# Performance work log

Hardware: AMD Instinct MI355X
Metric: run time of the kernel (lower is better)

## Reference

```python
import jax, jax.numpy as jnp
import numpy as np
from jax import lax

B, EMB, HEADS, HD, LAYERS, FIX, ADAPT, MLP, NCLS = 32, 768, 12, 64, 12, 6, 6, 3072, 100
PE_N, PE_D = 100, 256
SCALE = 1.0 / np.sqrt(HD)


def _ln(x, g, b, eps=1e-5):
    m = jnp.mean(x, axis=-1, keepdims=True)
    v = jnp.mean((x - m) ** 2, axis=-1, keepdims=True)
    return (x - m) / jnp.sqrt(v + eps) * g + b


def _vit_block(x, g1, b1, qkvw, qkvb, pw, pb, g2, b2, f1w, f1b, f2w, f2b):
    Bn, N, _ = x.shape
    h = _ln(x, g1, b1)
    qkv = (h @ qkvw + qkvb).reshape(Bn, N, 3, HEADS, HD)
    q, k, v = [qkv[:, :, i].transpose(0, 2, 1, 3) for i in range(3)]  # [B,H,N,hd]
    attn = jax.nn.softmax(jnp.einsum('bhqd,bhkd->bhqk', q, k) * SCALE, axis=-1)
    o = jnp.einsum('bhqk,bhkd->bhqd', attn, v).transpose(0, 2, 1, 3).reshape(Bn, N, EMB)
    x = x + (o @ pw + pb)
    h = _ln(x, g2, b2)
    return x + (jax.nn.gelu(h @ f1w + f1b, approximate=False) @ f2w + f2b)


def _sinusoid_table():
    pos = np.arange(PE_N)[:, None].astype(np.float64)
    j = np.arange(PE_D)[None, :]
    ang = pos / np.power(10000.0, 2 * (j // 2) / PE_D)
    tab = ang.copy()
    tab[:, 0::2] = np.sin(ang[:, 0::2])
    tab[:, 1::2] = np.cos(ang[:, 1::2])
    return jnp.asarray(tab, dtype=jnp.float32)


def setup_inputs() -> dict:
    key = jax.random.key(0)
    ks = iter(jax.random.split(key, 40))
    r = lambda shape: jax.random.normal(next(ks), shape, dtype=jnp.float32) * 0.02
    inp = {
        'x': jax.random.normal(next(ks), (B, 3, 224, 224), dtype=jnp.float32),
        'budget': jax.random.uniform(next(ks), (B,), dtype=jnp.float32),
        'pe_table': _sinusoid_table(),
        'lat_w1': r((PE_D, EMB)), 'lat_b1': r((EMB,)),
        'lat_ln_g': jnp.ones((EMB,), jnp.float32), 'lat_ln_b': jnp.zeros((EMB,), jnp.float32),
        'lat_w2': r((EMB, EMB)), 'lat_b2': r((EMB,)),
        'patch_w': r((EMB, 3, 16, 16)), 'patch_b': r((EMB,)),
        'cls_token': r((1, 1, EMB)), 'pos_embed': r((1, 198, EMB)),
        'sched_w': r((EMB, ADAPT)), 'sched_b': r((ADAPT,)),
        'ln1_g': jnp.ones((LAYERS, EMB), jnp.float32), 'ln1_b': jnp.zeros((LAYERS, EMB), jnp.float32),
        'qkv_w': r((LAYERS, EMB, 3 * EMB)), 'qkv_b': r((LAYERS, 3 * EMB)),
        'proj_w': r((LAYERS, EMB, EMB)), 'proj_b': r((LAYERS, EMB)),
        'ln2_g': jnp.ones((LAYERS, EMB), jnp.float32), 'ln2_b': jnp.zeros((LAYERS, EMB), jnp.float32),
        'fc1_w': r((LAYERS, EMB, MLP)), 'fc1_b': r((LAYERS, MLP)),
        'fc2_w': r((LAYERS, MLP, EMB)), 'fc2_b': r((LAYERS, EMB)),
        'norm_g': jnp.ones((EMB,), jnp.float32), 'norm_b': jnp.zeros((EMB,), jnp.float32),
        'head_w': r((EMB, NCLS)), 'head_b': r((NCLS,)),
    }
    return inp


def reference(x, budget, pe_table, lat_w1, lat_b1, lat_ln_g, lat_ln_b, lat_w2, lat_b2,
              patch_w, patch_b, cls_token, pos_embed, sched_w, sched_b,
              ln1_g, ln1_b, qkv_w, qkv_b, proj_w, proj_b, ln2_g, ln2_b,
              fc1_w, fc1_b, fc2_w, fc2_b, norm_g, norm_b, head_w, head_b):
    Bn = x.shape[0]
    bud = lax.stop_gradient(budget)
    # latency encoder
    idx = jnp.round(bud * (PE_N - 1)).astype(jnp.int32)
    h = pe_table[idx] @ lat_w1 + lat_b1
    h = jax.nn.gelu(h, approximate=False)
    h = _ln(h, lat_ln_g, lat_ln_b)
    lat = (h @ lat_w2 + lat_b2)[:, None, :]  # [B,1,EMB]
    # patch embed: conv16 s16 -> [B,EMB,14,14]
    p = lax.conv_general_dilated(x, patch_w, (16, 16), 'VALID',
                                 dimension_numbers=('NCHW', 'OIHW', 'NCHW'))
    p = (p + patch_b[None, :, None, None]).reshape(Bn, EMB, 196).transpose(0, 2, 1)
    tok = jnp.concatenate([lat, jnp.broadcast_to(cls_token, (Bn, 1, EMB)), p], axis=1)
    tok = tok + pos_embed  # [B,198,EMB]
    blk = lambda t, i: _vit_block(t, ln1_g[i], ln1_b[i], qkv_w[i], qkv_b[i], proj_w[i], proj_b[i],
                                  ln2_g[i], ln2_b[i], fc1_w[i], fc1_b[i], fc2_w[i], fc2_b[i])
    for i in range(FIX):
        tok = blk(tok, i)
    # layer routing (eval path): per-sample top-k over adaptive layers
    logits = tok[:, 0] @ sched_w + sched_b  # [B,ADAPT]
    k = jnp.maximum(jnp.ceil(bud * ADAPT).astype(jnp.int32), 1)  # [B]
    ranks = jnp.argsort(jnp.argsort(-logits, axis=-1), axis=-1)
    active = ranks < k[:, None]  # [B,ADAPT] bool
    t = tok[:, 1:]  # drop latency token -> [B,197,EMB]
    for i in range(ADAPT):
        out = blk(t, FIX + i)
        t = jnp.where(active[:, i, None, None], out, t)
    t = _ln(t, norm_g, norm_b)
    return t[:, 0] @ head_w + head_b
```

## Files before the change

### kernel.cpp

```cpp
#include <hip/hip_runtime.h>
#include <hip/hip_bf16.h>
#include <math.h>


using bf16   = __hip_bfloat16;
using short8 = __attribute__((ext_vector_type(8))) short;
using f32x4  = __attribute__((ext_vector_type(4))) float;

#define GLD16(gptr, lptr)                                                            \
    __builtin_amdgcn_global_load_lds((const __attribute__((address_space(1))) void*)(gptr), \
                                     (__attribute__((address_space(3))) void*)(lptr), 16, 0, 0)

__device__ __forceinline__ void split2(float x, short& h, short& l)
{
    unsigned u  = __float_as_uint(x);
    unsigned hr = (u + 0x7fffu + ((u >> 16) & 1u)) & 0xffff0000u;
    h = (short)(hr >> 16);
    float res = x - __uint_as_float(hr);
    l = (short)(__float_as_uint(res) >> 16);
}

__global__ __launch_bounds__(256) void trans_split_kernel(const float* __restrict__ W,
                                                          short* __restrict__ Wh,
                                                          short* __restrict__ Wl,
                                                          int K, int N)
{
    __shared__ float tile[32][33];
    int n0 = blockIdx.x * 32, k0 = blockIdx.y * 32;
    int c = threadIdx.x & 31, r = threadIdx.x >> 5;
    #pragma unroll
    for (int i = 0; i < 32; i += 8)
        tile[r + i][c] = W[(size_t)(k0 + r + i) * N + n0 + c];
    __syncthreads();
    #pragma unroll
    for (int i = 0; i < 32; i += 8) {
        short h, l; split2(tile[c][r + i], h, l);
        size_t o = (size_t)(n0 + r + i) * K + k0 + c;
        Wh[o] = h; Wl[o] = l;
    }
}

__global__ void split_kernel(const float* __restrict__ in, short* __restrict__ h,
                             short* __restrict__ l, int n)
{
    int i = blockIdx.x * 256 + threadIdx.x;
    if (i >= n) return;
    short hh, ll; split2(in[i], hh, ll);
    h[i] = hh; l[i] = ll;
}

__global__ void im2col_split_kernel(const float* __restrict__ x,
                                    short* __restrict__ Ah, short* __restrict__ Al)
{
    int idx = blockIdx.x * 256 + threadIdx.x;
    if (idx >= 6272 * 768) return;
    int k = idx % 768;
    int row = idx / 768;
    int b = row / 196, p = row % 196;
    int py = p / 14, px = p % 14;
    int c = k >> 8, rem = k & 255;
    int i = rem >> 4, j = rem & 15;
    float v = x[(((size_t)b * 3 + c) * 224 + py * 16 + i) * 224 + px * 16 + j];
    short h, l; split2(v, h, l);
    Ah[idx] = h; Al[idx] = l;
}

template<bool GELU, bool RES, bool SPLITOUT>
__global__ __launch_bounds__(256) void gemm3_kernel(const short* __restrict__ Ah,
                                                    const short* __restrict__ Al,
                                                    const short* __restrict__ Bh,
                                                    const short* __restrict__ Bl,
                                                    const float* __restrict__ bias,
                                                    const float* __restrict__ resid,
                                                    float* __restrict__ Cf,
                                                    short* __restrict__ Ch,
                                                    short* __restrict__ Cl,
                                                    int M, int N, int K)
{
    __shared__ __align__(16) short sm[2 * 4 * 128 * 32];
    const int tid  = threadIdx.x;
    const int lane = tid & 63;
    const int w    = tid >> 6;
    const int wm   = w >> 1, wn = w & 1;
    const int m0   = blockIdx.y * 128;
    const int n0   = blockIdx.x * 128;
    const int col  = lane & 15;
    const int quad = lane >> 4;
    const int srow = lane >> 2;
    const int skc  = (((lane & 3) ^ ((lane >> 3) & 3)) * 8);
    const int rswz = (quad ^ ((col >> 1) & 3)) * 8;

    f32x4 acc[4][4];
    #pragma unroll
    for (int i = 0; i < 4; ++i)
        #pragma unroll
        for (int j = 0; j < 4; ++j) acc[i][j] = (f32x4)0.f;

    const short* Ahb = Ah + (size_t)m0 * K;
    const short* Alb = Al + (size_t)m0 * K;
    const short* Bhb = Bh + (size_t)n0 * K;
    const short* Blb = Bl + (size_t)n0 * K;

    auto stage = [&](int buf, int t) {
        const int k0 = t << 5;
        short* dst = &sm[buf * 16384];
        #pragma unroll
        for (int i = 0; i < 2; ++i) {
            int r = w * 32 + i * 16;
            size_t go = (size_t)(r + srow) * K + k0 + skc;
            GLD16(Ahb + go, dst + r * 32);
            GLD16(Alb + go, dst + 4096 + r * 32);
            GLD16(Bhb + go, dst + 8192 + r * 32);
            GLD16(Blb + go, dst + 12288 + r * 32);
        }
    };

    auto compute = [&](int buf) {
        const short* cb = &sm[buf * 16384];
        short8 ah[4], al[4];
        #pragma unroll
        for (int mi = 0; mi < 4; ++mi) {
            int ao = (wm * 64 + mi * 16 + col) * 32 + rswz;
            ah[mi] = *(const short8*)(cb + ao);
            al[mi] = *(const short8*)(cb + 4096 + ao);
        }
        #pragma unroll
        for (int ni = 0; ni < 4; ++ni) {
            int bo = (wn * 64 + ni * 16 + col) * 32 + rswz;
            short8 bh = *(const short8*)(cb + 8192 + bo);
            short8 bl = *(const short8*)(cb + 12288 + bo);
            #pragma unroll
            for (int mi = 0; mi < 4; ++mi) {
                acc[mi][ni] = __builtin_amdgcn_mfma_f32_16x16x32_bf16(ah[mi], bh, acc[mi][ni], 0, 0, 0);
                acc[mi][ni] = __builtin_amdgcn_mfma_f32_16x16x32_bf16(al[mi], bh, acc[mi][ni], 0, 0, 0);
                acc[mi][ni] = __builtin_amdgcn_mfma_f32_16x16x32_bf16(ah[mi], bl, acc[mi][ni], 0, 0, 0);
            }
        }
    };

    const int nk = K >> 5;
    stage(0, 0);
    __syncthreads();
    int cur = 0;
    for (int t = 0; t < nk - 1; ++t) {
        stage(cur ^ 1, t + 1);
        compute(cur);
        __syncthreads();
        cur ^= 1;
    }
    compute(cur);

    #pragma unroll
    for (int mi = 0; mi < 4; ++mi) {
        #pragma unroll
        for (int ni = 0; ni < 4; ++ni) {
            int gcol = n0 + wn * 64 + ni * 16 + col;
            float bv = bias[gcol];
            #pragma unroll
            for (int r = 0; r < 4; ++r) {
                int grow = m0 + wm * 64 + mi * 16 + quad * 4 + r;
                if (grow < M) {
                    float v = acc[mi][ni][r] + bv;
                    if (RES) v += resid[(size_t)grow * N + gcol];
                    if (GELU) v = 0.5f * v * (1.f + erff(v * 0.70710678118654752f));
                    size_t o = (size_t)grow * N + gcol;
                    if (SPLITOUT) { short h, l; split2(v, h, l); Ch[o] = h; Cl[o] = l; }
                    else          Cf[o] = v;
                }
            }
        }
    }
}

__global__ __launch_bounds__(256) void ln_kernel(const float* __restrict__ x,
                                                 const float* __restrict__ g,
                                                 const float* __restrict__ bta,
                                                 short* __restrict__ outh,
                                                 short* __restrict__ outl, int M)
{
    int row = blockIdx.x * 4 + (threadIdx.x >> 6);
    int lane = threadIdx.x & 63;
    if (row >= M) return;
    const float* xr = x + (size_t)row * 768;
    float vals[12];
    float s = 0.f;
    #pragma unroll
    for (int i = 0; i < 12; ++i) { vals[i] = xr[lane + i * 64]; s += vals[i]; }
    #pragma unroll
    for (int off = 32; off; off >>= 1) s += __shfl_xor(s, off);
    float mean = s * (1.f / 768.f);
    float vs = 0.f;
    #pragma unroll
    for (int i = 0; i < 12; ++i) { float d = vals[i] - mean; vs += d * d; }
    #pragma unroll
    for (int off = 32; off; off >>= 1) vs += __shfl_xor(vs, off);
    float rstd = rsqrtf(vs * (1.f / 768.f) + 1e-5f);
    size_t rb = (size_t)row * 768;
    #pragma unroll
    for (int i = 0; i < 12; ++i) {
        int c = lane + i * 64;
        short h, l; split2((vals[i] - mean) * rstd * g[c] + bta[c], h, l);
        outh[rb + c] = h; outl[rb + c] = l;
    }
}

__global__ __launch_bounds__(128) void attn_kernel(const float* __restrict__ qkv,
                                                   short* __restrict__ Oh,
                                                   short* __restrict__ Ol, int S)
{
    __shared__ float Ks[64 * 64];
    __shared__ float Vs[64 * 64];
    int blk  = blockIdx.x;
    int bh   = blk >> 1, half = blk & 1;
    int b = bh / 12, h = bh % 12;
    int halfRows = (S + 1) >> 1;
    int q0   = half * halfRows;
    int qcnt = min(halfRows, S - q0);
    const float* base = qkv + (size_t)b * S * 2304;
    int tid = threadIdx.x;
    int r = q0 + tid;
    bool act = (tid < qcnt);
    float q[64];
    #pragma unroll
    for (int d = 0; d < 64; ++d) q[d] = 0.f;
    if (act) {
        const float4* qp = (const float4*)(base + (size_t)r * 2304 + h * 64);
        #pragma unroll
        for (int d4 = 0; d4 < 16; ++d4) {
            float4 t = qp[d4];
            q[4 * d4] = t.x; q[4 * d4 + 1] = t.y; q[4 * d4 + 2] = t.z; q[4 * d4 + 3] = t.w;
        }
    }
    float o[64];
    #pragma unroll
    for (int d = 0; d < 64; ++d) o[d] = 0.f;
    float m = -1e30f, l = 0.f;

    for (int jc = 0; jc < S; jc += 64) {
        int cnt = min(64, S - jc);
        __syncthreads();
        for (int idx = tid; idx < cnt * 16; idx += 128) {
            int j = idx >> 4, d4 = idx & 15;
            const float4* rp = (const float4*)(base + (size_t)(jc + j) * 2304 + h * 64) + d4;
            ((float4*)Ks)[j * 16 + d4] = rp[192];
            ((float4*)Vs)[j * 16 + d4] = rp[384];
        }
        __syncthreads();
        if (act) {
            for (int j0 = 0; j0 < cnt; j0 += 8) {
                float sc[8];
                float pm = -1e30f;
                #pragma unroll
                for (int jj = 0; jj < 8; ++jj) {
                    int j = j0 + jj;
                    const float4* kr = (const float4*)&Ks[j * 64];
                    float s0 = 0.f, s1 = 0.f, s2 = 0.f, s3 = 0.f;
                    #pragma unroll
                    for (int d4 = 0; d4 < 16; ++d4) {
                        float4 kv = kr[d4];
                        s0 += q[4 * d4]     * kv.x;
                        s1 += q[4 * d4 + 1] * kv.y;
                        s2 += q[4 * d4 + 2] * kv.z;
                        s3 += q[4 * d4 + 3] * kv.w;
                    }
                    float sv = ((s0 + s1) + (s2 + s3)) * 0.125f;
                    sv = (j < cnt) ? sv : -1e30f;
                    sc[jj] = sv;
                    pm = fmaxf(pm, sv);
                }
                if (!__all(pm <= m + 8.f)) {
                    float mn = fmaxf(m, pm);
                    float alpha = __expf(m - mn);
                    l *= alpha;
                    #pragma unroll
                    for (int d = 0; d < 64; ++d) o[d] *= alpha;
                    m = mn;
                }
                #pragma unroll
                for (int jj = 0; jj < 8; ++jj) {
                    float p = __expf(sc[jj] - m);
                    l += p;
                    const float4* vr = (const float4*)&Vs[(j0 + jj) * 64];
                    #pragma unroll
                    for (int d4 = 0; d4 < 16; ++d4) {
                        float4 vv = vr[d4];
                        o[4 * d4]     += p * vv.x;
                        o[4 * d4 + 1] += p * vv.y;
                        o[4 * d4 + 2] += p * vv.z;
                        o[4 * d4 + 3] += p * vv.w;
                    }
                }
            }
        }
    }
    if (act) {
        float inv = 1.f / l;
        size_t rb = (size_t)(b * S + r) * 768 + h * 64;
        #pragma unroll
        for (int d = 0; d < 64; ++d) {
            short hh, ll; split2(o[d] * inv, hh, ll);
            Oh[rb + d] = hh; Ol[rb + d] = ll;
        }
    }
}

__global__ __launch_bounds__(256) void latent1_kernel(const float* __restrict__ pe_table,
                                                      const float* __restrict__ budget,
                                                      const float* __restrict__ w1,
                                                      const float* __restrict__ b1,
                                                      float* __restrict__ hout)
{
    int b = blockIdx.x, tid = threadIdx.x;
    __shared__ float pe[256];
    int idx = (int)rintf(budget[b] * 99.f);
    pe[tid] = pe_table[idx * 256 + tid];
    __syncthreads();
    int col = blockIdx.y * 256 + tid;
    float a = b1[col];
    for (int k = 0; k < 256; ++k) a += pe[k] * w1[k * 768 + col];
    hout[b * 768 + col] = 0.5f * a * (1.f + erff(a * 0.70710678118654752f));
}

__global__ __launch_bounds__(256) void ln32_kernel(const float* __restrict__ x,
                                                   const float* __restrict__ g,
                                                   const float* __restrict__ bta,
                                                   float* __restrict__ outp)
{
    int row = blockIdx.x * 4 + (threadIdx.x >> 6);
    int lane = threadIdx.x & 63;
    const float* xr = x + (size_t)row * 768;
    float vals[12];
    float s = 0.f;
    #pragma unroll
    for (int i = 0; i < 12; ++i) { vals[i] = xr[lane + i * 64]; s += vals[i]; }
    #pragma unroll
    for (int off = 32; off; off >>= 1) s += __shfl_xor(s, off);
    float mean = s * (1.f / 768.f);
    float vs = 0.f;
    #pragma unroll
    for (int i = 0; i < 12; ++i) { float d = vals[i] - mean; vs += d * d; }
    #pragma unroll
    for (int off = 32; off; off >>= 1) vs += __shfl_xor(vs, off);
    float rstd = rsqrtf(vs * (1.f / 768.f) + 1e-5f);
    size_t rb = (size_t)row * 768;
    #pragma unroll
    for (int i = 0; i < 12; ++i) {
        int c = lane + i * 64;
        outp[rb + c] = (vals[i] - mean) * rstd * g[c] + bta[c];
    }
}

__global__ __launch_bounds__(256) void latent2_kernel(const float* __restrict__ hn,
                                                      const float* __restrict__ w2,
                                                      const float* __restrict__ b2,
                                                      float* __restrict__ lat)
{
    int b = blockIdx.x, tid = threadIdx.x;
    __shared__ float hrow[768];
    for (int i = tid; i < 768; i += 256) hrow[i] = hn[b * 768 + i];
    __syncthreads();
    int col = blockIdx.y * 256 + tid;
    float a = b2[col];
    for (int k = 0; k < 768; ++k) a += hrow[k] * w2[k * 768 + col];
    lat[b * 768 + col] = a;
}

__global__ void assemble_kernel(const float* __restrict__ lat, const float* __restrict__ cls,
                                const float* __restrict__ P, const float* __restrict__ pos,
                                float* __restrict__ T)
{
    int idx = blockIdx.x * 256 + threadIdx.x;
    if (idx >= 32 * 198 * 768) return;
    int c = idx % 768;
    int row = idx / 768;
    int b = row / 198, t = row % 198;
    float v;
    if (t == 0)      v = lat[b * 768 + c];
    else if (t == 1) v = cls[c];
    else             v = P[((size_t)b * 196 + (t - 2)) * 768 + c];
    T[idx] = v + pos[t * 768 + c];
}

__global__ void sched_kernel(const float* __restrict__ T, const float* __restrict__ sw,
                             const float* __restrict__ sb, const float* __restrict__ budget,
                             int* __restrict__ active)
{
    int b = blockIdx.x, lane = threadIdx.x;
    const float* xr = T + (size_t)b * 198 * 768;
    float acc[6] = {0, 0, 0, 0, 0, 0};
    for (int k = lane; k < 768; k += 64) {
        float xv = xr[k];
        #pragma unroll
        for (int i = 0; i < 6; ++i) acc[i] += xv * sw[k * 6 + i];
    }
    #pragma unroll
    for (int i = 0; i < 6; ++i)
        #pragma unroll
        for (int off = 32; off; off >>= 1) acc[i] += __shfl_xor(acc[i], off);
    if (lane == 0) {
        float lg[6];
        #pragma unroll
        for (int i = 0; i < 6; ++i) lg[i] = acc[i] + sb[i];
        int k = (int)ceilf(budget[b] * 6.f);
        if (k < 1) k = 1;
        for (int i = 0; i < 6; ++i) {
            int rank = 0;
            for (int j = 0; j < 6; ++j)
                rank += (lg[j] > lg[i]) || (lg[j] == lg[i] && j < i);
            active[b * 6 + i] = (rank < k) ? 1 : 0;
        }
    }
}

__global__ void droplat_kernel(const float* __restrict__ T, float* __restrict__ T2)
{
    int idx = blockIdx.x * 256 + threadIdx.x;
    if (idx >= 32 * 197 * 768) return;
    int c = idx % 768;
    int row = idx / 768;
    int b = row / 197, t = row % 197;
    T2[idx] = T[((size_t)b * 198 + t + 1) * 768 + c];
}

__global__ void select_kernel(float* __restrict__ T2, const float* __restrict__ OUT,
                              const int* __restrict__ active, int layer)
{
    int idx = blockIdx.x * 256 + threadIdx.x;
    if (idx >= 32 * 197 * 768) return;
    int b = idx / (197 * 768);
    if (active[b * 6 + layer]) T2[idx] = OUT[idx];
}

__global__ __launch_bounds__(128) void head_kernel(const float* __restrict__ T2,
                                                   const float* __restrict__ g,
                                                   const float* __restrict__ bta,
                                                   const float* __restrict__ hw,
                                                   const float* __restrict__ hb,
                                                   float* __restrict__ out)
{
    int b = blockIdx.x, tid = threadIdx.x;
    __shared__ float hn[768];
    __shared__ float red[128];
    const float* xr = T2 + (size_t)b * 197 * 768;
    float v[6];
    float s = 0.f;
    #pragma unroll
    for (int i = 0; i < 6; ++i) { v[i] = xr[tid + i * 128]; s += v[i]; }
    red[tid] = s; __syncthreads();
    for (int o = 64; o > 0; o >>= 1) { if (tid < o) red[tid] += red[tid + o]; __syncthreads(); }
    float mean = red[0] * (1.f / 768.f);
    __syncthreads();
    float vs = 0.f;
    #pragma unroll
    for (int i = 0; i < 6; ++i) { float d = v[i] - mean; vs += d * d; }
    red[tid] = vs; __syncthreads();
    for (int o = 64; o > 0; o >>= 1) { if (tid < o) red[tid] += red[tid + o]; __syncthreads(); }
    float rstd = rsqrtf(red[0] * (1.f / 768.f) + 1e-5f);
    #pragma unroll
    for (int i = 0; i < 6; ++i) {
        int c = tid + i * 128;
        hn[c] = (v[i] - mean) * rstd * g[c] + bta[c];
    }
    __syncthreads();
    if (tid < 100) {
        float a = hb[tid];
        for (int k = 0; k < 768; ++k) a += hn[k] * hw[k * 100 + tid];
        out[b * 100 + tid] = a;
    }
}

extern "C" void kernel_launch(void* const* d_in, const int* in_sizes, int n_in,
                              void* d_out, int out_size, void* d_ws, size_t ws_size,
                              hipStream_t stream)
{
    const float* x        = (const float*)d_in[0];
    const float* budget   = (const float*)d_in[1];
    const float* pe_table = (const float*)d_in[2];
    const float* lat_w1   = (const float*)d_in[3];
    const float* lat_b1   = (const float*)d_in[4];
    const float* lat_ln_g = (const float*)d_in[5];
    const float* lat_ln_b = (const float*)d_in[6];
    const float* lat_w2   = (const float*)d_in[7];
    const float* lat_b2   = (const float*)d_in[8];
    const float* patch_w  = (const float*)d_in[9];
    const float* patch_b  = (const float*)d_in[10];
    const float* cls_tok  = (const float*)d_in[11];
    const float* pos_emb  = (const float*)d_in[12];
    const float* sched_w  = (const float*)d_in[13];
    const float* sched_b  = (const float*)d_in[14];
    const float* ln1_g    = (const float*)d_in[15];
    const float* ln1_b    = (const float*)d_in[16];
    const float* qkv_w    = (const float*)d_in[17];
    const float* qkv_b    = (const float*)d_in[18];
    const float* proj_w   = (const float*)d_in[19];
    const float* proj_b   = (const float*)d_in[20];
    const float* ln2_g    = (const float*)d_in[21];
    const float* ln2_b    = (const float*)d_in[22];
    const float* fc1_w    = (const float*)d_in[23];
    const float* fc1_b    = (const float*)d_in[24];
    const float* fc2_w    = (const float*)d_in[25];
    const float* fc2_b    = (const float*)d_in[26];
    const float* norm_g   = (const float*)d_in[27];
    const float* norm_b   = (const float*)d_in[28];
    const float* head_w   = (const float*)d_in[29];
    const float* head_b   = (const float*)d_in[30];
    float* out = (float*)d_out;
    (void)in_sizes; (void)n_in; (void)out_size; (void)ws_size;

    char* ws = (char*)d_ws;
    size_t off = 0;
    auto alloc = [&](size_t bytes) -> char* {
        char* p = ws + off;
        off = (off + bytes + 255) & ~(size_t)255;
        return p;
    };
    short* sQKVh = (short*)alloc(2304ull * 768 * 2);
    short* sQKVl = (short*)alloc(2304ull * 768 * 2);
    short* sPRJh = (short*)alloc(768ull * 768 * 2);
    short* sPRJl = (short*)alloc(768ull * 768 * 2);
    short* sFC1h = (short*)alloc(3072ull * 768 * 2);
    short* sFC1l = (short*)alloc(3072ull * 768 * 2);
    short* sFC2h = (short*)alloc(768ull * 3072 * 2);
    short* sFC2l = (short*)alloc(768ull * 3072 * 2);
    short* pwh   = (short*)alloc(768ull * 768 * 2);
    short* pwl   = (short*)alloc(768ull * 768 * 2);
    float* T     = (float*)alloc(6400ull * 768 * 4);
    float* T2    = (float*)alloc(6400ull * 768 * 4);
    float* OUT   = (float*)alloc(6400ull * 768 * 4);
    short* Hh    = (short*)alloc(6400ull * 768 * 2);
    short* Hl    = (short*)alloc(6400ull * 768 * 2);
    float* QKV   = (float*)alloc(6336ull * 2304 * 4);
    short* Oh    = (short*)alloc(6400ull * 768 * 2);
    short* Ol    = (short*)alloc(6400ull * 768 * 2);
    short* Mh    = (short*)alloc(6400ull * 3072 * 2);
    short* Ml    = (short*)alloc(6400ull * 3072 * 2);
    float* lat   = (float*)alloc(32ull * 768 * 4);
    float* latH  = (float*)alloc(32ull * 768 * 4);
    float* latN  = (float*)alloc(32ull * 768 * 4);
    int*   act   = (int*)alloc(32 * 6 * 4);
    float* P     = QKV;
    short* Aph   = Mh;
    short* Apl   = Ml;

    im2col_split_kernel<<<(6272 * 768 + 255) / 256, 256, 0, stream>>>(x, Aph, Apl);
    split_kernel<<<(768 * 768 + 255) / 256, 256, 0, stream>>>(patch_w, pwh, pwl, 768 * 768);
    latent1_kernel<<<dim3(32, 3), 256, 0, stream>>>(pe_table, budget, lat_w1, lat_b1, latH);
    ln32_kernel<<<8, 256, 0, stream>>>(latH, lat_ln_g, lat_ln_b, latN);
    latent2_kernel<<<dim3(32, 3), 256, 0, stream>>>(latN, lat_w2, lat_b2, lat);
    gemm3_kernel<false, false, false><<<dim3(6, 49), 256, 0, stream>>>(
        Aph, Apl, pwh, pwl, patch_b, nullptr, P, nullptr, nullptr, 6272, 768, 768);
    assemble_kernel<<<(32 * 198 * 768 + 255) / 256, 256, 0, stream>>>(lat, cls_tok, P, pos_emb, T);

    for (int l = 0; l < 6; ++l) {
        trans_split_kernel<<<dim3(72, 24), 256, 0, stream>>>(qkv_w + (size_t)l * 768 * 2304, sQKVh, sQKVl, 768, 2304);
        trans_split_kernel<<<dim3(24, 24), 256, 0, stream>>>(proj_w + (size_t)l * 768 * 768, sPRJh, sPRJl, 768, 768);
        trans_split_kernel<<<dim3(96, 24), 256, 0, stream>>>(fc1_w + (size_t)l * 768 * 3072, sFC1h, sFC1l, 768, 3072);
        trans_split_kernel<<<dim3(24, 96), 256, 0, stream>>>(fc2_w + (size_t)l * 3072 * 768, sFC2h, sFC2l, 3072, 768);

        ln_kernel<<<6336 / 4, 256, 0, stream>>>(T, ln1_g + l * 768, ln1_b + l * 768, Hh, Hl, 6336);
        gemm3_kernel<false, false, false><<<dim3(18, 50), 256, 0, stream>>>(
            Hh, Hl, sQKVh, sQKVl, qkv_b + l * 2304, nullptr, QKV, nullptr, nullptr, 6336, 2304, 768);
        attn_kernel<<<768, 128, 0, stream>>>(QKV, Oh, Ol, 198);
        gemm3_kernel<false, true, false><<<dim3(6, 50), 256, 0, stream>>>(
            Oh, Ol, sPRJh, sPRJl, proj_b + l * 768, T, T, nullptr, nullptr, 6336, 768, 768);
        ln_kernel<<<6336 / 4, 256, 0, stream>>>(T, ln2_g + l * 768, ln2_b + l * 768, Hh, Hl, 6336);
        gemm3_kernel<true, false, true><<<dim3(24, 50), 256, 0, stream>>>(
            Hh, Hl, sFC1h, sFC1l, fc1_b + l * 3072, nullptr, nullptr, Mh, Ml, 6336, 3072, 768);
        gemm3_kernel<false, true, false><<<dim3(6, 50), 256, 0, stream>>>(
            Mh, Ml, sFC2h, sFC2l, fc2_b + l * 768, T, T, nullptr, nullptr, 6336, 768, 3072);
    }

    sched_kernel<<<32, 64, 0, stream>>>(T, sched_w, sched_b, budget, act);
    droplat_kernel<<<(32 * 197 * 768 + 255) / 256, 256, 0, stream>>>(T, T2);

    for (int i = 0; i < 6; ++i) {
        int l = 6 + i;
        trans_split_kernel<<<dim3(72, 24), 256, 0, stream>>>(qkv_w + (size_t)l * 768 * 2304, sQKVh, sQKVl, 768, 2304);
        trans_split_kernel<<<dim3(24, 24), 256, 0, stream>>>(proj_w + (size_t)l * 768 * 768, sPRJh, sPRJl, 768, 768);
        trans_split_kernel<<<dim3(96, 24), 256, 0, stream>>>(fc1_w + (size_t)l * 768 * 3072, sFC1h, sFC1l, 768, 3072);
        trans_split_kernel<<<dim3(24, 96), 256, 0, stream>>>(fc2_w + (size_t)l * 3072 * 768, sFC2h, sFC2l, 3072, 768);

        ln_kernel<<<6304 / 4, 256, 0, stream>>>(T2, ln1_g + l * 768, ln1_b + l * 768, Hh, Hl, 6304);
        gemm3_kernel<false, false, false><<<dim3(18, 50), 256, 0, stream>>>(
            Hh, Hl, sQKVh, sQKVl, qkv_b + l * 2304, nullptr, QKV, nullptr, nullptr, 6304, 2304, 768);
        attn_kernel<<<768, 128, 0, stream>>>(QKV, Oh, Ol, 197);
        gemm3_kernel<false, true, false><<<dim3(6, 50), 256, 0, stream>>>(
            Oh, Ol, sPRJh, sPRJl, proj_b + l * 768, T2, OUT, nullptr, nullptr, 6304, 768, 768);
        ln_kernel<<<6304 / 4, 256, 0, stream>>>(OUT, ln2_g + l * 768, ln2_b + l * 768, Hh, Hl, 6304);
        gemm3_kernel<true, false, true><<<dim3(24, 50), 256, 0, stream>>>(
            Hh, Hl, sFC1h, sFC1l, fc1_b + l * 3072, nullptr, nullptr, Mh, Ml, 6304, 3072, 768);
        gemm3_kernel<false, true, false><<<dim3(6, 50), 256, 0, stream>>>(
            Mh, Ml, sFC2h, sFC2l, fc2_b + l * 768, OUT, OUT, nullptr, nullptr, 6304, 768, 3072);
        select_kernel<<<(32 * 197 * 768 + 255) / 256, 256, 0, stream>>>(T2, OUT, act, i);
    }

    head_kernel<<<32, 128, 0, stream>>>(T2, norm_g, norm_b, head_w, head_b, out);
}
```

Baseline: 7.284 ms.

## Add 128x64 GEMM tile for N=768 GEMMs and XCD-aware workgroup remapping

Templates the split-bf16 GEMM on the N tile width and adds a 128x64 variant, where each wave covers 32 rows by 64 columns. The N=768 GEMMs (patch embed, proj, fc2) use it, doubling their grid from 300 to 600 workgroups so the many CUs are better filled. It also remaps workgroup IDs so consecutive tiles land on the same XCD, aiming for better L2 reuse. The narrower tile lowers per-block operand reuse and puts more pressure on LDS and global traffic.

```diff
diff --git a/kernel.cpp b/kernel.cpp
--- a/kernel.cpp
+++ b/kernel.cpp
@@ -65,7 +65,7 @@
     Ah[idx] = h; Al[idx] = l;
 }
 
-template<bool GELU, bool RES, bool SPLITOUT>
+template<int BN, bool GELU, bool RES, bool SPLITOUT>
 __global__ __launch_bounds__(256) void gemm3_kernel(const short* __restrict__ Ah,
                                                     const short* __restrict__ Al,
                                                     const short* __restrict__ Bh,
@@ -77,22 +77,36 @@
                                                     short* __restrict__ Cl,
                                                     int M, int N, int K)
 {
-    __shared__ __align__(16) short sm[2 * 4 * 128 * 32];
+    constexpr int AL_OFF = 4096;
+    constexpr int BH_OFF = 8192;
+    constexpr int BL_OFF = 8192 + BN * 32;
+    constexpr int BUFSZ  = 8192 + BN * 64;
+    constexpr int MI     = (BN == 128) ? 4 : 2;
+    __shared__ __align__(16) short sm[2 * BUFSZ];
     const int tid  = threadIdx.x;
     const int lane = tid & 63;
     const int w    = tid >> 6;
-    const int wm   = w >> 1, wn = w & 1;
-    const int m0   = blockIdx.y * 128;
-    const int n0   = blockIdx.x * 128;
+    const int wm   = (BN == 128) ? (w >> 1) : w;
+    const int wn   = (BN == 128) ? (w & 1) : 0;
+
+    const int gx  = gridDim.x;
+    const int nwg = gx * gridDim.y;
+    const int wg  = blockIdx.y * gx + blockIdx.x;
+    const int qq  = nwg >> 3, rr = nwg & 7;
+    const int xcd = wg & 7, seq = wg >> 3;
+    const int work = (xcd < rr ? xcd * (qq + 1) : rr * (qq + 1) + (xcd - rr) * qq) + seq;
+    const int m0   = (work / gx) * 128;
+    const int n0   = (work % gx) * BN;
+
     const int col  = lane & 15;
     const int quad = lane >> 4;
     const int srow = lane >> 2;
     const int skc  = (((lane & 3) ^ ((lane >> 3) & 3)) * 8);
     const int rswz = (quad ^ ((col >> 1) & 3)) * 8;
 
-    f32x4 acc[4][4];
-    #pragma unroll
-    for (int i = 0; i < 4; ++i)
+    f32x4 acc[MI][4];
+    #pragma unroll
+    for (int i = 0; i < MI; ++i)
         #pragma unroll
         for (int j = 0; j < 4; ++j) acc[i][j] = (f32x4)0.f;
 
@@ -103,34 +117,42 @@
 
     auto stage = [&](int buf, int t) {
         const int k0 = t << 5;
-        short* dst = &sm[buf * 16384];
+        short* dst = &sm[buf * BUFSZ];
         #pragma unroll
         for (int i = 0; i < 2; ++i) {
             int r = w * 32 + i * 16;
             size_t go = (size_t)(r + srow) * K + k0 + skc;
             GLD16(Ahb + go, dst + r * 32);
-            GLD16(Alb + go, dst + 4096 + r * 32);
-            GLD16(Bhb + go, dst + 8192 + r * 32);
-            GLD16(Blb + go, dst + 12288 + r * 32);
+            GLD16(Alb + go, dst + AL_OFF + r * 32);
+            if (BN == 128) {
+                GLD16(Bhb + go, dst + BH_OFF + r * 32);
+                GLD16(Blb + go, dst + BL_OFF + r * 32);
+            }
+        }
+        if (BN == 64) {
+            int r = w * 16;
+            size_t go = (size_t)(r + srow) * K + k0 + skc;
+            GLD16(Bhb + go, dst + BH_OFF + r * 32);
+            GLD16(Blb + go, dst + BL_OFF + r * 32);
         }
     };
 
     auto compute = [&](int buf) {
-        const short* cb = &sm[buf * 16384];
-        short8 ah[4], al[4];
-        #pragma unroll
-        for (int mi = 0; mi < 4; ++mi) {
-            int ao = (wm * 64 + mi * 16 + col) * 32 + rswz;
+        const short* cb = &sm[buf * BUFSZ];
+        short8 ah[MI], al[MI];
+        #pragma unroll
+        for (int mi = 0; mi < MI; ++mi) {
+            int ao = (wm * (MI * 16) + mi * 16 + col) * 32 + rswz;
             ah[mi] = *(const short8*)(cb + ao);
-            al[mi] = *(const short8*)(cb + 4096 + ao);
+            al[mi] = *(const short8*)(cb + AL_OFF + ao);
         }
         #pragma unroll
         for (int ni = 0; ni < 4; ++ni) {
-            int bo = (wn * 64 + ni * 16 + col) * 32 + rswz;
-            short8 bh = *(const short8*)(cb + 8192 + bo);
-            short8 bl = *(const short8*)(cb + 12288 + bo);
+            int bo = ((BN == 128 ? wn * 64 : 0) + ni * 16 + col) * 32 + rswz;
+            short8 bh = *(const short8*)(cb + BH_OFF + bo);
+            short8 bl = *(const short8*)(cb + BL_OFF + bo);
             #pragma unroll
-            for (int mi = 0; mi < 4; ++mi) {
+            for (int mi = 0; mi < MI; ++mi) {
                 acc[mi][ni] = __builtin_amdgcn_mfma_f32_16x16x32_bf16(ah[mi], bh, acc[mi][ni], 0, 0, 0);
                 acc[mi][ni] = __builtin_amdgcn_mfma_f32_16x16x32_bf16(al[mi], bh, acc[mi][ni], 0, 0, 0);
                 acc[mi][ni] = __builtin_amdgcn_mfma_f32_16x16x32_bf16(ah[mi], bl, acc[mi][ni], 0, 0, 0);
@@ -151,14 +173,14 @@
     compute(cur);
 
     #pragma unroll
-    for (int mi = 0; mi < 4; ++mi) {
+    for (int mi = 0; mi < MI; ++mi) {
         #pragma unroll
         for (int ni = 0; ni < 4; ++ni) {
-            int gcol = n0 + wn * 64 + ni * 16 + col;
+            int gcol = n0 + (BN == 128 ? wn * 64 : 0) + ni * 16 + col;
             float bv = bias[gcol];
             #pragma unroll
             for (int r = 0; r < 4; ++r) {
-                int grow = m0 + wm * 64 + mi * 16 + quad * 4 + r;
+                int grow = m0 + wm * (MI * 16) + mi * 16 + quad * 4 + r;
                 if (grow < M) {
                     float v = acc[mi][ni][r] + bv;
                     if (RES) v += resid[(size_t)grow * N + gcol];
@@ -547,7 +569,7 @@
     latent1_kernel<<<dim3(32, 3), 256, 0, stream>>>(pe_table, budget, lat_w1, lat_b1, latH);
     ln32_kernel<<<8, 256, 0, stream>>>(latH, lat_ln_g, lat_ln_b, latN);
     latent2_kernel<<<dim3(32, 3), 256, 0, stream>>>(latN, lat_w2, lat_b2, lat);
-    gemm3_kernel<false, false, false><<<dim3(6, 49), 256, 0, stream>>>(
+    gemm3_kernel<64, false, false, false><<<dim3(12, 49), 256, 0, stream>>>(
         Aph, Apl, pwh, pwl, patch_b, nullptr, P, nullptr, nullptr, 6272, 768, 768);
     assemble_kernel<<<(32 * 198 * 768 + 255) / 256, 256, 0, stream>>>(lat, cls_tok, P, pos_emb, T);
 
@@ -558,15 +580,15 @@
         trans_split_kernel<<<dim3(24, 96), 256, 0, stream>>>(fc2_w + (size_t)l * 3072 * 768, sFC2h, sFC2l, 3072, 768);
 
         ln_kernel<<<6336 / 4, 256, 0, stream>>>(T, ln1_g + l * 768, ln1_b + l * 768, Hh, Hl, 6336);
-        gemm3_kernel<false, false, false><<<dim3(18, 50), 256, 0, stream>>>(
+        gemm3_kernel<128, false, false, false><<<dim3(18, 50), 256, 0, stream>>>(
             Hh, Hl, sQKVh, sQKVl, qkv_b + l * 2304, nullptr, QKV, nullptr, nullptr, 6336, 2304, 768);
         attn_kernel<<<768, 128, 0, stream>>>(QKV, Oh, Ol, 198);
-        gemm3_kernel<false, true, false><<<dim3(6, 50), 256, 0, stream>>>(
+        gemm3_kernel<64, false, true, false><<<dim3(12, 50), 256, 0, stream>>>(
             Oh, Ol, sPRJh, sPRJl, proj_b + l * 768, T, T, nullptr, nullptr, 6336, 768, 768);
         ln_kernel<<<6336 / 4, 256, 0, stream>>>(T, ln2_g + l * 768, ln2_b + l * 768, Hh, Hl, 6336);
-        gemm3_kernel<true, false, true><<<dim3(24, 50), 256, 0, stream>>>(
+        gemm3_kernel<128, true, false, true><<<dim3(24, 50), 256, 0, stream>>>(
             Hh, Hl, sFC1h, sFC1l, fc1_b + l * 3072, nullptr, nullptr, Mh, Ml, 6336, 3072, 768);
-        gemm3_kernel<false, true, false><<<dim3(6, 50), 256, 0, stream>>>(
+        gemm3_kernel<64, false, true, false><<<dim3(12, 50), 256, 0, stream>>>(
             Mh, Ml, sFC2h, sFC2l, fc2_b + l * 768, T, T, nullptr, nullptr, 6336, 768, 3072);
     }
 
@@ -581,15 +603,15 @@
         trans_split_kernel<<<dim3(24, 96), 256, 0, stream>>>(fc2_w + (size_t)l * 3072 * 768, sFC2h, sFC2l, 3072, 768);
 
         ln_kernel<<<6304 / 4, 256, 0, stream>>>(T2, ln1_g + l * 768, ln1_b + l * 768, Hh, Hl, 6304);
-        gemm3_kernel<false, false, false><<<dim3(18, 50), 256, 0, stream>>>(
+        gemm3_kernel<128, false, false, false><<<dim3(18, 50), 256, 0, stream>>>(
             Hh, Hl, sQKVh, sQKVl, qkv_b + l * 2304, nullptr, QKV, nullptr, nullptr, 6304, 2304, 768);
         attn_kernel<<<768, 128, 0, stream>>>(QKV, Oh, Ol, 197);
-        gemm3_kernel<false, true, false><<<dim3(6, 50), 256, 0, stream>>>(
+        gemm3_kernel<64, false, true, false><<<dim3(12, 50), 256, 0, stream>>>(
             Oh, Ol, sPRJh, sPRJl, proj_b + l * 768, T2, OUT, nullptr, nullptr, 6304, 768, 768);
         ln_kernel<<<6304 / 4, 256, 0, stream>>>(OUT, ln2_g + l * 768, ln2_b + l * 768, Hh, Hl, 6304);
-        gemm3_kernel<true, false, true><<<dim3(24, 50), 256, 0, stream>>>(
+        gemm3_kernel<128, true, false, true><<<dim3(24, 50), 256, 0, stream>>>(
             Hh, Hl, sFC1h, sFC1l, fc1_b + l * 3072, nullptr, nullptr, Mh, Ml, 6304, 3072, 768);
-        gemm3_kernel<false, true, false><<<dim3(6, 50), 256, 0, stream>>>(
+        gemm3_kernel<64, false, true, false><<<dim3(12, 50), 256, 0, stream>>>(
             Mh, Ml, sFC2h, sFC2l, fc2_b + l * 768, OUT, OUT, nullptr, nullptr, 6304, 768, 3072);
         select_kernel<<<(32 * 197 * 768 + 255) / 256, 256, 0, stream>>>(T2, OUT, act, i);
     }
```

After: 7.029 ms. 3.5% less time.
